# Performance work log

Hardware: AMD Instinct MI355X
Metric: run time of the kernel (lower is better)

Reference implementation:

```python
import jax, jax.numpy as jnp
import numpy as np

B, LQ, LV, D = 16, 2048, 2048, 1024


def setup_inputs() -> dict:
    key = jax.random.key(0)
    kq, kv = jax.random.split(key)
    query = jax.random.normal(kq, (B, LQ, D), dtype=jnp.float32)
    value = jax.random.normal(kv, (B, LV, D), dtype=jnp.float32)
    return {"query": query, "value": value}


def reference(query, value):
    # score: [B, Lq, Lv] -- unscaled dot-product attention (no 1/sqrt(d))
    score = jnp.einsum('bqd,bvd->bqv', query, value)
    attn = jax.nn.softmax(score, axis=-1)
    # dropout is identity in eval mode
    context = jnp.einsum('bqv,bvd->bqd', attn, value)
    return context
```

## Files before the change

kernel.cpp:

```cpp
#include <hip/hip_runtime.h>


#define B_ 16
#define LQ_ 2048
#define LV_ 2048
#define DD_ 1024

typedef unsigned short u16;
typedef _Float16 f16x8 __attribute__((ext_vector_type(8)));
typedef __attribute__((ext_vector_type(4))) float f32x4;
typedef __attribute__((ext_vector_type(4))) unsigned short u16x4;

__device__ __forceinline__ u16 f2h(float x) {
  union { _Float16 h; u16 u; } c;
  c.h = (_Float16)x;
  return c.u;
}

__device__ __forceinline__ void gload16(const u16* g, u16* lds) {
  __builtin_amdgcn_global_load_lds(
      (const __attribute__((address_space(1))) void*)g,
      (__attribute__((address_space(3))) void*)lds, 16, 0, 0);
}

#define BARRIER() do { asm volatile("" ::: "memory"); __builtin_amdgcn_s_barrier(); asm volatile("" ::: "memory"); } while (0)
#define WAITVM(N) asm volatile("s_waitcnt vmcnt(" #N ")" ::: "memory")

template <int TPS, int MODE>
__global__ __launch_bounds__(512, 2) void k_gemm8(
    const u16* __restrict__ A, const u16* __restrict__ B,
    u16* __restrict__ Pout, float* __restrict__ Fout,
    const u16* __restrict__ r2tab,
    float* __restrict__ mtab, float* __restrict__ stab,
    int N, int lda, int ldb, size_t aBatch, size_t bBatch, size_t cBatch) {
  constexpr int NT = TPS;
  __shared__ u16 lds[65536];
  __shared__ u16 ldsR2[(MODE == 2) ? 8192 : 64];
  u16* ldsA = lds;
  u16* ldsB = lds + 32768;

  int bx, by, bz;
  {
    const int gx = gridDim.x, gy = gridDim.y;
    const int lid = blockIdx.x + gx * (blockIdx.y + gy * blockIdx.z);
    const int nwg = gx * gy * gridDim.z;
    const int q = nwg >> 3;
    const int nid = (lid & 7) * q + (lid >> 3);
    bx = nid % gx;
    const int rem = nid / gx;
    by = rem % gy;
    bz = rem / gy;
  }

  const int tid = threadIdx.x;
  const int w = tid >> 6, l = tid & 63;
  const int m0 = by << 8, n0 = bx << 8;
  const int wr = w >> 2, wc = w & 3;
  const int wr128 = wr * 128, wc64 = wc * 64;
  const int fr = l & 15, kx = l >> 4, fr7 = l & 7, cc = l & 15;
  const int srow = l >> 3;
  const int gsrc8 = (((l & 7) ^ ((l >> 3) & 7)) << 3);

  const u16* Ab = A + (size_t)bz * aBatch;
  const u16* Bb = B + (size_t)bz * bBatch;

  if constexpr (MODE == 2) {
    for (int i = tid; i < 8192; i += 512)
      ldsR2[i] = r2tab[((size_t)bz * 32 + (i >> 8)) * 2048 + m0 + (i & 255)];
    __syncthreads();
  }

#define STAGE_A(tt, h)                                                          \
  do {                                                                          \
    const int kk_ = (tt) * 64;                                                  \
    u16* d0_ = ldsA + ((tt) & 1) * 16384 + ((h) * 64 + w * 8) * 64;             \
    const u16* g0_ = Ab + (size_t)(m0 + (h) * 64 + w * 8 + srow) * lda + kk_ + gsrc8; \
    gload16(g0_, d0_);                                                          \
    gload16(g0_ + (size_t)128 * lda, d0_ + 128 * 64);                           \
  } while (0)

#define STAGE_B(tt, h)                                                          \
  do {                                                                          \
    const int kk_ = (tt) * 64;                                                  \
    const int rb_ = (w >> 2) * 64 + (h) * 32 + (w & 3) * 8;                     \
    u16* d0_ = ldsB + ((tt) & 1) * 16384 + rb_ * 64;                            \
    const u16* g0_ = Bb + (size_t)(n0 + rb_ + srow) * ldb + kk_ + gsrc8;        \
    gload16(g0_, d0_);                                                          \
    gload16(g0_ + (size_t)128 * ldb, d0_ + 8192);                               \
  } while (0)

#define RA8(MOFF)                                                                   \
  {                                                                                 \
    _Pragma("unroll") for (int m_ = 0; m_ < 4; ++m_) {                              \
      _Pragma("unroll") for (int k_ = 0; k_ < 2; ++k_) {                            \
        af[m_][k_] = *(const f16x8*)(ldsA + bufo +                                  \
            (wr128 + (MOFF) + m_ * 16 + fr) * 64 + (((kx + k_ * 4) ^ fr7) << 3));   \
        if constexpr (MODE == 2) af[m_][k_] = af[m_][k_] * r2h[(MOFF) / 16 + m_];   \
      }                                                                             \
    }                                                                               \
  }

#define RB4(NF0)                                                                    \
  {                                                                                 \
    _Pragma("unroll") for (int n_ = 0; n_ < 2; ++n_) {                              \
      _Pragma("unroll") for (int k_ = 0; k_ < 2; ++k_) {                            \
        bf[(NF0) + n_][k_] = *(const f16x8*)(ldsB + bufo +                          \
            (wc64 + ((NF0) + n_) * 16 + fr) * 64 + (((kx + k_ * 4) ^ fr7) << 3));   \
      }                                                                             \
    }                                                                               \
  }

#define MFMA8(MF0, NF0)                                                             \
  {                                                                                 \
    _Pragma("unroll") for (int m_ = 0; m_ < 4; ++m_)                                \
    _Pragma("unroll") for (int n_ = 0; n_ < 2; ++n_)                                \
    _Pragma("unroll") for (int k_ = 0; k_ < 2; ++k_)                                \
        acc[(MF0) + m_][(NF0) + n_] = __builtin_amdgcn_mfma_f32_16x16x32_f16(       \
            af[m_][k_], bf[(NF0) + n_][k_], acc[(MF0) + m_][(NF0) + n_], 0, 0, 0);  \
  }

  f32x4 acc[8][4];
#pragma unroll
  for (int i = 0; i < 8; ++i)
#pragma unroll
    for (int j = 0; j < 4; ++j) acc[i][j] = (f32x4){0.f, 0.f, 0.f, 0.f};
  f16x8 af[4][2], bf[4][2];
  _Float16 r2h[8];

  STAGE_A(0, 0); STAGE_A(0, 1); STAGE_B(0, 0); STAGE_B(0, 1);
  STAGE_A(1, 0); STAGE_B(1, 0); STAGE_A(1, 1);
  WAITVM(6);
  BARRIER();

#pragma unroll 2
  for (int t = 0; t < NT; ++t) {
    const int bufo = (t & 1) * 16384;
    if constexpr (MODE == 2) {
#pragma unroll
      for (int i = 0; i < 8; ++i)
        r2h[i] = *(const _Float16*)&ldsR2[t * 256 + wr128 + i * 16 + fr];
    }
    RA8(0);
    RB4(0);
    if (t + 1 < NT) STAGE_B(t + 1, 1);
    BARRIER();
    __builtin_amdgcn_s_setprio(1); MFMA8(0, 0); __builtin_amdgcn_s_setprio(0);
    BARRIER();
    RB4(2);
    if (t + 2 < NT) STAGE_A(t + 2, 0);
    BARRIER();
    __builtin_amdgcn_s_setprio(1); MFMA8(0, 2); __builtin_amdgcn_s_setprio(0);
    BARRIER();
    RA8(64);
    if (t + 2 < NT) STAGE_B(t + 2, 0);
    BARRIER();
    __builtin_amdgcn_s_setprio(1); MFMA8(4, 0); __builtin_amdgcn_s_setprio(0);
    BARRIER();
    if (t + 2 < NT) STAGE_A(t + 2, 1);
    BARRIER();
    __builtin_amdgcn_s_setprio(1); MFMA8(4, 2); __builtin_amdgcn_s_setprio(0);
    if (t + 2 < NT) { WAITVM(6); } else if (t + 1 < NT) { WAITVM(0); }
    BARRIER();
  }

  const int rg4 = (l >> 4) * 4;
  if constexpr (MODE == 1) {
    u16* Pc = Pout + (size_t)bz * ((size_t)2048 * 2048);
    const int chunk = bx * 4 + wc;
    const size_t tbase = ((size_t)bz * 32 + chunk) * 2048 + m0;
#pragma unroll
    for (int mf = 0; mf < 8; ++mf) {
      float mt4[4], st4[4];
#pragma unroll
      for (int j = 0; j < 4; ++j) {
        const int r_ = wr128 + mf * 16 + rg4 + j;
        float v = fmaxf(fmaxf(acc[mf][0][j], acc[mf][1][j]),
                        fmaxf(acc[mf][2][j], acc[mf][3][j]));
#pragma unroll
        for (int off = 1; off < 16; off <<= 1) v = fmaxf(v, __shfl_xor(v, off, 64));
        const float e0 = __expf(acc[mf][0][j] - v);
        const float e1 = __expf(acc[mf][1][j] - v);
        const float e2 = __expf(acc[mf][2][j] - v);
        const float e3 = __expf(acc[mf][3][j] - v);
        u16* pr = Pc + (size_t)(m0 + r_) * 2048 + n0 + wc64 + cc;
        pr[0] = f2h(e0);
        pr[16] = f2h(e1);
        pr[32] = f2h(e2);
        pr[48] = f2h(e3);
        float s = (e0 + e1) + (e2 + e3);
#pragma unroll
        for (int off = 1; off < 16; off <<= 1) s += __shfl_xor(s, off, 64);
        mt4[j] = v;
        st4[j] = s;
      }
      if ((l & 15) == 0) {
        const int r0 = wr128 + mf * 16 + rg4;
        *(float4*)&mtab[tbase + r0] = make_float4(mt4[0], mt4[1], mt4[2], mt4[3]);
        *(float4*)&stab[tbase + r0] = make_float4(st4[0], st4[1], st4[2], st4[3]);
      }
    }
  } else {
#pragma unroll
    for (int mf = 0; mf < 8; ++mf)
#pragma unroll
      for (int nf = 0; nf < 4; ++nf) {
        float* cp = Fout + (size_t)bz * cBatch +
                    (size_t)(m0 + wr128 + mf * 16 + rg4) * N + n0 + wc64 + nf * 16 + cc;
#pragma unroll
        for (int j = 0; j < 4; ++j)
          cp[(size_t)j * N] = acc[mf][nf][j];
      }
  }
#undef STAGE_A
#undef STAGE_B
#undef RA8
#undef RB4
#undef MFMA8
}

__global__ __launch_bounds__(256) void k_stats(const float* __restrict__ mtab,
                                               const float* __restrict__ stab,
                                               u16* __restrict__ r2tab) {
  const int r = blockIdx.x * 256 + threadIdx.x;
  const int bz = blockIdx.y;
  float m[32], s[32], mg = -3.0e38f;
#pragma unroll
  for (int t = 0; t < 32; ++t) {
    m[t] = mtab[((size_t)bz * 32 + t) * 2048 + r];
    s[t] = stab[((size_t)bz * 32 + t) * 2048 + r];
    mg = fmaxf(mg, m[t]);
  }
  float denom = 0.f;
  float f[32];
#pragma unroll
  for (int t = 0; t < 32; ++t) {
    f[t] = __expf(m[t] - mg);
    denom += s[t] * f[t];
  }
  const float inv = 1.0f / denom;
#pragma unroll
  for (int t = 0; t < 32; ++t)
    r2tab[((size_t)bz * 32 + t) * 2048 + r] = f2h(f[t] * inv);
}

__global__ __launch_bounds__(256) void k_conv_q(const float* __restrict__ in,
                                                u16* __restrict__ hi_o, int nrows) {
  int t = blockIdx.x * 256 + threadIdx.x;
  int total = nrows * (DD_ / 4);
  if (t >= total) return;
  int row = t >> 8;
  int c4 = (t & 255) << 2;
  float4 v = *(const float4*)(in + (size_t)row * DD_ + c4);
  u16x4 hi;
  hi.x = f2h(v.x);
  hi.y = f2h(v.y);
  hi.z = f2h(v.z);
  hi.w = f2h(v.w);
  *(u16x4*)(hi_o + (size_t)row * DD_ + c4) = hi;
}

__global__ __launch_bounds__(256) void k_conv_vt(const float* __restrict__ V,
                                                 u16* __restrict__ Vh,
                                                 u16* __restrict__ VT) {
  __shared__ u16 tile[64][65];
  const int d0 = blockIdx.x * 64, v0 = blockIdx.y * 64;
  const size_t boff = (size_t)blockIdx.z * LV_ * DD_;
  const float* Vb = V + boff;
  u16* Vhb = Vh + boff;
  u16* VTb = VT + (size_t)blockIdx.z * DD_ * LV_;
  const int t = threadIdx.x;
  const int r = t >> 4, c4 = (t & 15) * 4;
#pragma unroll
  for (int i = 0; i < 4; ++i) {
    int row = r + i * 16;
    float4 x = *(const float4*)(Vb + (size_t)(v0 + row) * DD_ + d0 + c4);
    u16x4 h;
    h.x = f2h(x.x);
    h.y = f2h(x.y);
    h.z = f2h(x.z);
    h.w = f2h(x.w);
    *(u16x4*)(Vhb + (size_t)(v0 + row) * DD_ + d0 + c4) = h;
    tile[row][c4 + 0] = h.x;
    tile[row][c4 + 1] = h.y;
    tile[row][c4 + 2] = h.z;
    tile[row][c4 + 3] = h.w;
  }
  __syncthreads();
#pragma unroll
  for (int i = 0; i < 4; ++i) {
    int row = r + i * 16;
    u16x4 o;
    o.x = tile[c4 + 0][row];
    o.y = tile[c4 + 1][row];
    o.z = tile[c4 + 2][row];
    o.w = tile[c4 + 3][row];
    *(u16x4*)(VTb + (size_t)(d0 + row) * LV_ + v0 + c4) = o;
  }
}

extern "C" void kernel_launch(void* const* d_in, const int* in_sizes, int n_in,
                              void* d_out, int out_size, void* d_ws, size_t ws_size,
                              hipStream_t stream) {
  const float* Q = (const float*)d_in[0];
  const float* V = (const float*)d_in[1];
  float* out = (float*)d_out;

  const size_t qv_e = (size_t)LQ_ * DD_;
  const size_t vt_e = (size_t)DD_ * LV_;
  const size_t p_e = (size_t)LQ_ * LV_;
  const size_t tab_e = (size_t)32 * 2048;
  const size_t per_batch =
      qv_e * 2 * 2 + vt_e * 2 + p_e * 2 + tab_e * 4 * 2 + tab_e * 2;

  int nb = (int)(ws_size / per_batch);
  if (nb < 1) nb = 1;
  if (nb > B_) nb = B_;

  char* wp = (char*)d_ws;
  u16* Qh = (u16*)wp;    wp += (size_t)nb * qv_e * 2;
  u16* Vh = (u16*)wp;    wp += (size_t)nb * qv_e * 2;
  u16* VT = (u16*)wp;    wp += (size_t)nb * vt_e * 2;
  u16* P = (u16*)wp;     wp += (size_t)nb * p_e * 2;
  float* mtab = (float*)wp;  wp += (size_t)nb * tab_e * 4;
  float* stab = (float*)wp;  wp += (size_t)nb * tab_e * 4;
  u16* r2tab = (u16*)wp;

  for (int b0 = 0; b0 < B_; b0 += nb) {
    const int cb = (nb < B_ - b0) ? nb : (B_ - b0);
    const int rows = cb * LQ_;
    const int cthreads = rows * (DD_ / 4);
    k_conv_q<<<dim3((cthreads + 255) / 256), dim3(256), 0, stream>>>(
        Q + (size_t)b0 * LQ_ * DD_, Qh, rows);
    k_conv_vt<<<dim3(DD_ / 64, LV_ / 64, cb), dim3(256), 0, stream>>>(
        V + (size_t)b0 * LV_ * DD_, Vh, VT);
    k_gemm8<16, 1><<<dim3(LV_ / 256, LQ_ / 256, cb), dim3(512), 0, stream>>>(
        Qh, Vh, P, nullptr, nullptr, mtab, stab,
        LV_, DD_, DD_, qv_e, qv_e, 0);
    k_stats<<<dim3(LQ_ / 256, cb), dim3(256), 0, stream>>>(mtab, stab, r2tab);
    k_gemm8<32, 2><<<dim3(DD_ / 256, LQ_ / 256, cb), dim3(512), 0, stream>>>(
        P, VT, nullptr, out + (size_t)b0 * LQ_ * DD_, r2tab, nullptr, nullptr,
        DD_, LV_, LV_, p_e, vt_e, (size_t)LQ_ * DD_);
  }
}
```

Baseline: 416.1 us.

## Make GEMM workgroups loop over multiple N tiles with batch-per-XCD mapping

Each GEMM workgroup now walks several consecutive N tiles (4 for QK^T, 2 for PV) in one continuous K pipeline, running the softmax or store epilogue and clearing the accumulators at each tile boundary. Both launches shrink to a 2x8x16 grid. A new block mapping places whole batches on the same XCD, so A tiles and B panels stay in the local L2. The cost is half as many workgroups, so each CU may run only one 512-thread block instead of two, and the epilogue now sits inside the main loop where it can stall the pipeline.

```diff
diff --git a/kernel.cpp b/kernel.cpp
--- a/kernel.cpp
+++ b/kernel.cpp
@@ -26,35 +26,38 @@
 #define BARRIER() do { asm volatile("" ::: "memory"); __builtin_amdgcn_s_barrier(); asm volatile("" ::: "memory"); } while (0)
 #define WAITVM(N) asm volatile("s_waitcnt vmcnt(" #N ")" ::: "memory")
 
-template <int TPS, int MODE>
+template <int TPW, int TPS, int MODE>
 __global__ __launch_bounds__(512, 2) void k_gemm8(
     const u16* __restrict__ A, const u16* __restrict__ B,
     u16* __restrict__ Pout, float* __restrict__ Fout,
     const u16* __restrict__ r2tab,
     float* __restrict__ mtab, float* __restrict__ stab,
     int N, int lda, int ldb, size_t aBatch, size_t bBatch, size_t cBatch) {
-  constexpr int NT = TPS;
+  constexpr int NT = TPW * TPS;
   __shared__ u16 lds[65536];
   __shared__ u16 ldsR2[(MODE == 2) ? 8192 : 64];
   u16* ldsA = lds;
   u16* ldsB = lds + 32768;
 
   int bx, by, bz;
-  {
-    const int gx = gridDim.x, gy = gridDim.y;
-    const int lid = blockIdx.x + gx * (blockIdx.y + gy * blockIdx.z);
-    const int nwg = gx * gy * gridDim.z;
-    const int q = nwg >> 3;
-    const int nid = (lid & 7) * q + (lid >> 3);
-    bx = nid % gx;
-    const int rem = nid / gx;
-    by = rem % gy;
-    bz = rem / gy;
+  if (gridDim.z == 16 && gridDim.x == 2 && gridDim.y == 8) {
+    const int lid = blockIdx.x + 2 * (blockIdx.y + 8 * blockIdx.z);
+    const int xcd = lid & 7;
+    const int j = lid >> 3;
+    bz = xcd * 2 + (j >> 4);
+    const int r = j & 15;
+    by = r & 7;
+    bx = r >> 3;
+  } else {
+    bx = blockIdx.x;
+    by = blockIdx.y;
+    bz = blockIdx.z;
   }
 
   const int tid = threadIdx.x;
   const int w = tid >> 6, l = tid & 63;
-  const int m0 = by << 8, n0 = bx << 8;
+  const int m0 = by << 8;
+  const int n0base = bx * (TPW * 256);
   const int wr = w >> 2, wc = w & 3;
   const int wr128 = wr * 128, wc64 = wc * 64;
   const int fr = l & 15, kx = l >> 4, fr7 = l & 7, cc = l & 15;
@@ -72,7 +75,7 @@
 
 #define STAGE_A(tt, h)                                                          \
   do {                                                                          \
-    const int kk_ = (tt) * 64;                                                  \
+    const int kk_ = ((tt) % TPS) * 64;                                          \
     u16* d0_ = ldsA + ((tt) & 1) * 16384 + ((h) * 64 + w * 8) * 64;             \
     const u16* g0_ = Ab + (size_t)(m0 + (h) * 64 + w * 8 + srow) * lda + kk_ + gsrc8; \
     gload16(g0_, d0_);                                                          \
@@ -81,10 +84,11 @@
 
 #define STAGE_B(tt, h)                                                          \
   do {                                                                          \
-    const int kk_ = (tt) * 64;                                                  \
+    const int kk_ = ((tt) % TPS) * 64;                                          \
+    const int nb_ = n0base + ((tt) / TPS) * 256;                                \
     const int rb_ = (w >> 2) * 64 + (h) * 32 + (w & 3) * 8;                     \
     u16* d0_ = ldsB + ((tt) & 1) * 16384 + rb_ * 64;                            \
-    const u16* g0_ = Bb + (size_t)(n0 + rb_ + srow) * ldb + kk_ + gsrc8;        \
+    const u16* g0_ = Bb + (size_t)(nb_ + rb_ + srow) * ldb + kk_ + gsrc8;       \
     gload16(g0_, d0_);                                                          \
     gload16(g0_ + (size_t)128 * ldb, d0_ + 8192);                               \
   } while (0)
@@ -127,6 +131,8 @@
   f16x8 af[4][2], bf[4][2];
   _Float16 r2h[8];
 
+  const int rg4 = (l >> 4) * 4;
+
   STAGE_A(0, 0); STAGE_A(0, 1); STAGE_B(0, 0); STAGE_B(0, 1);
   STAGE_A(1, 0); STAGE_B(1, 0); STAGE_A(1, 1);
   WAITVM(6);
@@ -136,9 +142,10 @@
   for (int t = 0; t < NT; ++t) {
     const int bufo = (t & 1) * 16384;
     if constexpr (MODE == 2) {
+      const int chb = (t & (TPS - 1)) * 256;
 #pragma unroll
       for (int i = 0; i < 8; ++i)
-        r2h[i] = *(const _Float16*)&ldsR2[t * 256 + wr128 + i * 16 + fr];
+        r2h[i] = *(const _Float16*)&ldsR2[chb + wr128 + i * 16 + fr];
     }
     RA8(0);
     RB4(0);
@@ -161,55 +168,61 @@
     __builtin_amdgcn_s_setprio(1); MFMA8(4, 2); __builtin_amdgcn_s_setprio(0);
     if (t + 2 < NT) { WAITVM(6); } else if (t + 1 < NT) { WAITVM(0); }
     BARRIER();
-  }
-
-  const int rg4 = (l >> 4) * 4;
-  if constexpr (MODE == 1) {
-    u16* Pc = Pout + (size_t)bz * ((size_t)2048 * 2048);
-    const int chunk = bx * 4 + wc;
-    const size_t tbase = ((size_t)bz * 32 + chunk) * 2048 + m0;
-#pragma unroll
-    for (int mf = 0; mf < 8; ++mf) {
-      float mt4[4], st4[4];
-#pragma unroll
-      for (int j = 0; j < 4; ++j) {
-        const int r_ = wr128 + mf * 16 + rg4 + j;
-        float v = fmaxf(fmaxf(acc[mf][0][j], acc[mf][1][j]),
-                        fmaxf(acc[mf][2][j], acc[mf][3][j]));
-#pragma unroll
-        for (int off = 1; off < 16; off <<= 1) v = fmaxf(v, __shfl_xor(v, off, 64));
-        const float e0 = __expf(acc[mf][0][j] - v);
-        const float e1 = __expf(acc[mf][1][j] - v);
-        const float e2 = __expf(acc[mf][2][j] - v);
-        const float e3 = __expf(acc[mf][3][j] - v);
-        u16* pr = Pc + (size_t)(m0 + r_) * 2048 + n0 + wc64 + cc;
-        pr[0] = f2h(e0);
-        pr[16] = f2h(e1);
-        pr[32] = f2h(e2);
-        pr[48] = f2h(e3);
-        float s = (e0 + e1) + (e2 + e3);
-#pragma unroll
-        for (int off = 1; off < 16; off <<= 1) s += __shfl_xor(s, off, 64);
-        mt4[j] = v;
-        st4[j] = s;
+
+    if ((t & (TPS - 1)) == (TPS - 1)) {
+      const int n0c = n0base + (t / TPS) * 256;
+      if constexpr (MODE == 1) {
+        u16* Pc = Pout + (size_t)bz * ((size_t)2048 * 2048);
+        const int chunk = (n0c >> 6) + wc;
+        const size_t tbase = ((size_t)bz * 32 + chunk) * 2048 + m0;
+#pragma unroll
+        for (int mf = 0; mf < 8; ++mf) {
+          float mt4[4], st4[4];
+#pragma unroll
+          for (int j = 0; j < 4; ++j) {
+            const int r_ = wr128 + mf * 16 + rg4 + j;
+            float v = fmaxf(fmaxf(acc[mf][0][j], acc[mf][1][j]),
+                            fmaxf(acc[mf][2][j], acc[mf][3][j]));
+#pragma unroll
+            for (int off = 1; off < 16; off <<= 1) v = fmaxf(v, __shfl_xor(v, off, 64));
+            const float e0 = __expf(acc[mf][0][j] - v);
+            const float e1 = __expf(acc[mf][1][j] - v);
+            const float e2 = __expf(acc[mf][2][j] - v);
+            const float e3 = __expf(acc[mf][3][j] - v);
+            u16* pr = Pc + (size_t)(m0 + r_) * 2048 + n0c + wc64 + cc;
+            pr[0] = f2h(e0);
+            pr[16] = f2h(e1);
+            pr[32] = f2h(e2);
+            pr[48] = f2h(e3);
+            float s = (e0 + e1) + (e2 + e3);
+#pragma unroll
+            for (int off = 1; off < 16; off <<= 1) s += __shfl_xor(s, off, 64);
+            mt4[j] = v;
+            st4[j] = s;
+          }
+          if ((l & 15) == 0) {
+            const int r0 = wr128 + mf * 16 + rg4;
+            *(float4*)&mtab[tbase + r0] = make_float4(mt4[0], mt4[1], mt4[2], mt4[3]);
+            *(float4*)&stab[tbase + r0] = make_float4(st4[0], st4[1], st4[2], st4[3]);
+          }
+        }
+      } else {
+#pragma unroll
+        for (int mf = 0; mf < 8; ++mf)
+#pragma unroll
+          for (int nf = 0; nf < 4; ++nf) {
+            float* cp = Fout + (size_t)bz * cBatch +
+                        (size_t)(m0 + wr128 + mf * 16 + rg4) * N + n0c + wc64 + nf * 16 + cc;
+#pragma unroll
+            for (int j = 0; j < 4; ++j)
+              cp[(size_t)j * N] = acc[mf][nf][j];
+          }
       }
-      if ((l & 15) == 0) {
-        const int r0 = wr128 + mf * 16 + rg4;
-        *(float4*)&mtab[tbase + r0] = make_float4(mt4[0], mt4[1], mt4[2], mt4[3]);
-        *(float4*)&stab[tbase + r0] = make_float4(st4[0], st4[1], st4[2], st4[3]);
-      }
+#pragma unroll
+      for (int i = 0; i < 8; ++i)
+#pragma unroll
+        for (int j = 0; j < 4; ++j) acc[i][j] = (f32x4){0.f, 0.f, 0.f, 0.f};
     }
-  } else {
-#pragma unroll
-    for (int mf = 0; mf < 8; ++mf)
-#pragma unroll
-      for (int nf = 0; nf < 4; ++nf) {
-        float* cp = Fout + (size_t)bz * cBatch +
-                    (size_t)(m0 + wr128 + mf * 16 + rg4) * N + n0 + wc64 + nf * 16 + cc;
-#pragma unroll
-        for (int j = 0; j < 4; ++j)
-          cp[(size_t)j * N] = acc[mf][nf][j];
-      }
   }
 #undef STAGE_A
 #undef STAGE_B
@@ -333,11 +346,11 @@
         Q + (size_t)b0 * LQ_ * DD_, Qh, rows);
     k_conv_vt<<<dim3(DD_ / 64, LV_ / 64, cb), dim3(256), 0, stream>>>(
         V + (size_t)b0 * LV_ * DD_, Vh, VT);
-    k_gemm8<16, 1><<<dim3(LV_ / 256, LQ_ / 256, cb), dim3(512), 0, stream>>>(
+    k_gemm8<4, 16, 1><<<dim3(2, 8, cb), dim3(512), 0, stream>>>(
         Qh, Vh, P, nullptr, nullptr, mtab, stab,
         LV_, DD_, DD_, qv_e, qv_e, 0);
     k_stats<<<dim3(LQ_ / 256, cb), dim3(256), 0, stream>>>(mtab, stab, r2tab);
-    k_gemm8<32, 2><<<dim3(DD_ / 256, LQ_ / 256, cb), dim3(512), 0, stream>>>(
+    k_gemm8<2, 32, 2><<<dim3(2, 8, cb), dim3(512), 0, stream>>>(
         P, VT, nullptr, out + (size_t)b0 * LQ_ * DD_, r2tab, nullptr, nullptr,
         DD_, LV_, LV_, p_e, vt_e, (size_t)LQ_ * DD_);
   }
```

Measured after the change: 431.3 us. 1.04x slower.

## Replace pipelined 256x256 GEMM with simple 128x128 single-buffered GEMM

Applied to the files above, without the earlier changes.

Replaces the 512-thread, 256x256-tile GEMM with a 256-thread, 128x128-tile GEMM. The old kernel double-buffered 64-wide K slabs, interleaved loads with MFMA phases and raised wave priority around the MFMAs. The new kernel stages 32-wide K slabs through a single LDS buffer with two __syncthreads per step and a new XOR swizzle, and launches at 4 blocks per CU. The smaller tile and LDS footprint aim to raise occupancy and simplify the code. In exchange it gives up load/compute overlap and halves per-block data reuse, so it needs more global traffic and synchronisation per FLOP.

```diff
diff --git a/kernel.cpp b/kernel.cpp
--- a/kernel.cpp
+++ b/kernel.cpp
@@ -23,21 +23,16 @@
       (__attribute__((address_space(3))) void*)lds, 16, 0, 0);
 }
 
-#define BARRIER() do { asm volatile("" ::: "memory"); __builtin_amdgcn_s_barrier(); asm volatile("" ::: "memory"); } while (0)
-#define WAITVM(N) asm volatile("s_waitcnt vmcnt(" #N ")" ::: "memory")
-
-template <int TPS, int MODE>
-__global__ __launch_bounds__(512, 2) void k_gemm8(
+template <int K, int MODE>
+__global__ __launch_bounds__(256, 4) void k_gemm(
     const u16* __restrict__ A, const u16* __restrict__ B,
     u16* __restrict__ Pout, float* __restrict__ Fout,
     const u16* __restrict__ r2tab,
     float* __restrict__ mtab, float* __restrict__ stab,
     int N, int lda, int ldb, size_t aBatch, size_t bBatch, size_t cBatch) {
-  constexpr int NT = TPS;
-  __shared__ u16 lds[65536];
-  __shared__ u16 ldsR2[(MODE == 2) ? 8192 : 64];
-  u16* ldsA = lds;
-  u16* ldsB = lds + 32768;
+  __shared__ u16 ldsA[128 * 32];
+  __shared__ u16 ldsB[128 * 32];
+  __shared__ u16 ldsR2[(MODE == 2) ? (K / 64) * 128 : 64];
 
   int bx, by, bz;
   {
@@ -54,126 +49,78 @@
 
   const int tid = threadIdx.x;
   const int w = tid >> 6, l = tid & 63;
-  const int m0 = by << 8, n0 = bx << 8;
-  const int wr = w >> 2, wc = w & 3;
-  const int wr128 = wr * 128, wc64 = wc * 64;
-  const int fr = l & 15, kx = l >> 4, fr7 = l & 7, cc = l & 15;
-  const int srow = l >> 3;
-  const int gsrc8 = (((l & 7) ^ ((l >> 3) & 7)) << 3);
+  const int m0 = by << 7, n0 = bx << 7;
+  const int wr64 = (w >> 1) * 64, wc64 = (w & 1) * 64;
+  const int fr = l & 15, kx = l >> 4;
+  const int rg4 = kx * 4, cc = fr;
+  const int gsw = ((kx ^ ((fr ^ (fr >> 2)) & 3)) << 3);
+  const int rd = tid >> 2, gd = tid & 3;
+  const int gsA0 = ((gd ^ ((rd ^ (rd >> 2)) & 3)) << 3);
+  const int rd1 = rd + 64;
+  const int gsA1 = ((gd ^ ((rd1 ^ (rd1 >> 2)) & 3)) << 3);
 
   const u16* Ab = A + (size_t)bz * aBatch;
   const u16* Bb = B + (size_t)bz * bBatch;
 
   if constexpr (MODE == 2) {
-    for (int i = tid; i < 8192; i += 512)
-      ldsR2[i] = r2tab[((size_t)bz * 32 + (i >> 8)) * 2048 + m0 + (i & 255)];
+    for (int i = tid; i < (K / 64) * 128; i += 256)
+      ldsR2[i] = r2tab[((size_t)bz * 32 + (i >> 7)) * 2048 + m0 + (i & 127)];
     __syncthreads();
   }
 
-#define STAGE_A(tt, h)                                                          \
-  do {                                                                          \
-    const int kk_ = (tt) * 64;                                                  \
-    u16* d0_ = ldsA + ((tt) & 1) * 16384 + ((h) * 64 + w * 8) * 64;             \
-    const u16* g0_ = Ab + (size_t)(m0 + (h) * 64 + w * 8 + srow) * lda + kk_ + gsrc8; \
-    gload16(g0_, d0_);                                                          \
-    gload16(g0_ + (size_t)128 * lda, d0_ + 128 * 64);                           \
-  } while (0)
-
-#define STAGE_B(tt, h)                                                          \
-  do {                                                                          \
-    const int kk_ = (tt) * 64;                                                  \
-    const int rb_ = (w >> 2) * 64 + (h) * 32 + (w & 3) * 8;                     \
-    u16* d0_ = ldsB + ((tt) & 1) * 16384 + rb_ * 64;                            \
-    const u16* g0_ = Bb + (size_t)(n0 + rb_ + srow) * ldb + kk_ + gsrc8;        \
-    gload16(g0_, d0_);                                                          \
-    gload16(g0_ + (size_t)128 * ldb, d0_ + 8192);                               \
-  } while (0)
-
-#define RA8(MOFF)                                                                   \
-  {                                                                                 \
-    _Pragma("unroll") for (int m_ = 0; m_ < 4; ++m_) {                              \
-      _Pragma("unroll") for (int k_ = 0; k_ < 2; ++k_) {                            \
-        af[m_][k_] = *(const f16x8*)(ldsA + bufo +                                  \
-            (wr128 + (MOFF) + m_ * 16 + fr) * 64 + (((kx + k_ * 4) ^ fr7) << 3));   \
-        if constexpr (MODE == 2) af[m_][k_] = af[m_][k_] * r2h[(MOFF) / 16 + m_];   \
-      }                                                                             \
-    }                                                                               \
-  }
-
-#define RB4(NF0)                                                                    \
-  {                                                                                 \
-    _Pragma("unroll") for (int n_ = 0; n_ < 2; ++n_) {                              \
-      _Pragma("unroll") for (int k_ = 0; k_ < 2; ++k_) {                            \
-        bf[(NF0) + n_][k_] = *(const f16x8*)(ldsB + bufo +                          \
-            (wc64 + ((NF0) + n_) * 16 + fr) * 64 + (((kx + k_ * 4) ^ fr7) << 3));   \
-      }                                                                             \
-    }                                                                               \
-  }
-
-#define MFMA8(MF0, NF0)                                                             \
-  {                                                                                 \
-    _Pragma("unroll") for (int m_ = 0; m_ < 4; ++m_)                                \
-    _Pragma("unroll") for (int n_ = 0; n_ < 2; ++n_)                                \
-    _Pragma("unroll") for (int k_ = 0; k_ < 2; ++k_)                                \
-        acc[(MF0) + m_][(NF0) + n_] = __builtin_amdgcn_mfma_f32_16x16x32_f16(       \
-            af[m_][k_], bf[(NF0) + n_][k_], acc[(MF0) + m_][(NF0) + n_], 0, 0, 0);  \
-  }
-
-  f32x4 acc[8][4];
-#pragma unroll
-  for (int i = 0; i < 8; ++i)
+  f32x4 acc[4][4];
+#pragma unroll
+  for (int i = 0; i < 4; ++i)
 #pragma unroll
     for (int j = 0; j < 4; ++j) acc[i][j] = (f32x4){0.f, 0.f, 0.f, 0.f};
-  f16x8 af[4][2], bf[4][2];
-  _Float16 r2h[8];
-
-  STAGE_A(0, 0); STAGE_A(0, 1); STAGE_B(0, 0); STAGE_B(0, 1);
-  STAGE_A(1, 0); STAGE_B(1, 0); STAGE_A(1, 1);
-  WAITVM(6);
-  BARRIER();
-
-#pragma unroll 2
-  for (int t = 0; t < NT; ++t) {
-    const int bufo = (t & 1) * 16384;
+  f16x8 af[4], bf[4];
+  _Float16 r2h[4];
+
+  for (int kt = 0; kt < K; kt += 32) {
+    {
+      const u16* ga = Ab + (size_t)(m0 + rd) * lda + kt;
+      const u16* gb = Bb + (size_t)(n0 + rd) * ldb + kt;
+      gload16(ga + gsA0, &ldsA[rd * 32 + gd * 8]);
+      gload16(ga + (size_t)64 * lda + gsA1, &ldsA[rd1 * 32 + gd * 8]);
+      gload16(gb + gsA0, &ldsB[rd * 32 + gd * 8]);
+      gload16(gb + (size_t)64 * ldb + gsA1, &ldsB[rd1 * 32 + gd * 8]);
+    }
+    __syncthreads();
     if constexpr (MODE == 2) {
-#pragma unroll
-      for (int i = 0; i < 8; ++i)
-        r2h[i] = *(const _Float16*)&ldsR2[t * 256 + wr128 + i * 16 + fr];
-    }
-    RA8(0);
-    RB4(0);
-    if (t + 1 < NT) STAGE_B(t + 1, 1);
-    BARRIER();
-    __builtin_amdgcn_s_setprio(1); MFMA8(0, 0); __builtin_amdgcn_s_setprio(0);
-    BARRIER();
-    RB4(2);
-    if (t + 2 < NT) STAGE_A(t + 2, 0);
-    BARRIER();
-    __builtin_amdgcn_s_setprio(1); MFMA8(0, 2); __builtin_amdgcn_s_setprio(0);
-    BARRIER();
-    RA8(64);
-    if (t + 2 < NT) STAGE_B(t + 2, 0);
-    BARRIER();
-    __builtin_amdgcn_s_setprio(1); MFMA8(4, 0); __builtin_amdgcn_s_setprio(0);
-    BARRIER();
-    if (t + 2 < NT) STAGE_A(t + 2, 1);
-    BARRIER();
-    __builtin_amdgcn_s_setprio(1); MFMA8(4, 2); __builtin_amdgcn_s_setprio(0);
-    if (t + 2 < NT) { WAITVM(6); } else if (t + 1 < NT) { WAITVM(0); }
-    BARRIER();
-  }
-
-  const int rg4 = (l >> 4) * 4;
+      if ((kt & 63) == 0) {
+        const int chb = (kt >> 6) * 128;
+#pragma unroll
+        for (int m_ = 0; m_ < 4; ++m_)
+          r2h[m_] = *(const _Float16*)&ldsR2[chb + wr64 + m_ * 16 + fr];
+      }
+    }
+#pragma unroll
+    for (int m_ = 0; m_ < 4; ++m_) {
+      af[m_] = *(const f16x8*)&ldsA[(wr64 + m_ * 16 + fr) * 32 + gsw];
+      if constexpr (MODE == 2) af[m_] = af[m_] * r2h[m_];
+    }
+#pragma unroll
+    for (int n_ = 0; n_ < 4; ++n_)
+      bf[n_] = *(const f16x8*)&ldsB[(wc64 + n_ * 16 + fr) * 32 + gsw];
+#pragma unroll
+    for (int m_ = 0; m_ < 4; ++m_)
+#pragma unroll
+      for (int n_ = 0; n_ < 4; ++n_)
+        acc[m_][n_] = __builtin_amdgcn_mfma_f32_16x16x32_f16(
+            af[m_], bf[n_], acc[m_][n_], 0, 0, 0);
+    __syncthreads();
+  }
+
   if constexpr (MODE == 1) {
     u16* Pc = Pout + (size_t)bz * ((size_t)2048 * 2048);
-    const int chunk = bx * 4 + wc;
+    const int chunk = bx * 2 + (w & 1);
     const size_t tbase = ((size_t)bz * 32 + chunk) * 2048 + m0;
 #pragma unroll
-    for (int mf = 0; mf < 8; ++mf) {
+    for (int mf = 0; mf < 4; ++mf) {
       float mt4[4], st4[4];
 #pragma unroll
       for (int j = 0; j < 4; ++j) {
-        const int r_ = wr128 + mf * 16 + rg4 + j;
+        const int r_ = wr64 + mf * 16 + rg4 + j;
         float v = fmaxf(fmaxf(acc[mf][0][j], acc[mf][1][j]),
                         fmaxf(acc[mf][2][j], acc[mf][3][j]));
 #pragma unroll
@@ -194,28 +141,22 @@
         st4[j] = s;
       }
       if ((l & 15) == 0) {
-        const int r0 = wr128 + mf * 16 + rg4;
+        const int r0 = wr64 + mf * 16 + rg4;
         *(float4*)&mtab[tbase + r0] = make_float4(mt4[0], mt4[1], mt4[2], mt4[3]);
         *(float4*)&stab[tbase + r0] = make_float4(st4[0], st4[1], st4[2], st4[3]);
       }
     }
   } else {
-#pragma unroll
-    for (int mf = 0; mf < 8; ++mf)
+    float* Cb = Fout + (size_t)bz * cBatch;
+#pragma unroll
+    for (int mf = 0; mf < 4; ++mf)
 #pragma unroll
       for (int nf = 0; nf < 4; ++nf) {
-        float* cp = Fout + (size_t)bz * cBatch +
-                    (size_t)(m0 + wr128 + mf * 16 + rg4) * N + n0 + wc64 + nf * 16 + cc;
-#pragma unroll
-        for (int j = 0; j < 4; ++j)
-          cp[(size_t)j * N] = acc[mf][nf][j];
-      }
-  }
-#undef STAGE_A
-#undef STAGE_B
-#undef RA8
-#undef RB4
-#undef MFMA8
+        float* cp = Cb + (size_t)(m0 + wr64 + mf * 16 + rg4) * N + n0 + wc64 + nf * 16 + cc;
+#pragma unroll
+        for (int j = 0; j < 4; ++j) cp[(size_t)j * N] = acc[mf][nf][j];
+      }
+  }
 }
 
 __global__ __launch_bounds__(256) void k_stats(const float* __restrict__ mtab,
@@ -333,11 +274,11 @@
         Q + (size_t)b0 * LQ_ * DD_, Qh, rows);
     k_conv_vt<<<dim3(DD_ / 64, LV_ / 64, cb), dim3(256), 0, stream>>>(
         V + (size_t)b0 * LV_ * DD_, Vh, VT);
-    k_gemm8<16, 1><<<dim3(LV_ / 256, LQ_ / 256, cb), dim3(512), 0, stream>>>(
+    k_gemm<1024, 1><<<dim3(LV_ / 128, LQ_ / 128, cb), dim3(256), 0, stream>>>(
         Qh, Vh, P, nullptr, nullptr, mtab, stab,
         LV_, DD_, DD_, qv_e, qv_e, 0);
     k_stats<<<dim3(LQ_ / 256, cb), dim3(256), 0, stream>>>(mtab, stab, r2tab);
-    k_gemm8<32, 2><<<dim3(DD_ / 256, LQ_ / 256, cb), dim3(512), 0, stream>>>(
+    k_gemm<2048, 2><<<dim3(DD_ / 128, LQ_ / 128, cb), dim3(256), 0, stream>>>(
         P, VT, nullptr, out + (size_t)b0 * LQ_ * DD_, r2tab, nullptr, nullptr,
         DD_, LV_, LV_, p_e, vt_e, (size_t)LQ_ * DD_);
   }
```

Measured after the change: 455.9 us. 9.6% more time.

## Fuse softmax stats into second GEMM and make first GEMM persistent over two M tiles

Applied to the files above, without the earlier changes.

Removes the separate k_stats kernel: the second GEMM's prologue now reduces the per-chunk max and sum tables directly into LDS rescale factors. The first GEMM is restructured so each workgroup walks two consecutive 256-row M tiles, with the epilogue moved inside the loop so it runs at each tile boundary and staging continues across tiles. This cuts a kernel launch and the r2tab round trip, and lets the pipeline stay primed between tiles. The cost is fewer workgroups for the first GEMM and serial per-row work by 256 threads in each second-GEMM workgroup prologue. The fp16 round trip of the factors before multiplying by inv may change rounding slightly.

```diff
diff --git a/kernel.cpp b/kernel.cpp
--- a/kernel.cpp
+++ b/kernel.cpp
@@ -16,6 +16,11 @@
   c.h = (_Float16)x;
   return c.u;
 }
+__device__ __forceinline__ float h2f(u16 u) {
+  union { _Float16 h; u16 u; } c;
+  c.u = u;
+  return (float)c.h;
+}
 
 __device__ __forceinline__ void gload16(const u16* g, u16* lds) {
   __builtin_amdgcn_global_load_lds(
@@ -26,14 +31,13 @@
 #define BARRIER() do { asm volatile("" ::: "memory"); __builtin_amdgcn_s_barrier(); asm volatile("" ::: "memory"); } while (0)
 #define WAITVM(N) asm volatile("s_waitcnt vmcnt(" #N ")" ::: "memory")
 
-template <int TPS, int MODE>
+template <int TPW, int TPS, int MODE>
 __global__ __launch_bounds__(512, 2) void k_gemm8(
     const u16* __restrict__ A, const u16* __restrict__ B,
     u16* __restrict__ Pout, float* __restrict__ Fout,
-    const u16* __restrict__ r2tab,
     float* __restrict__ mtab, float* __restrict__ stab,
     int N, int lda, int ldb, size_t aBatch, size_t bBatch, size_t cBatch) {
-  constexpr int NT = TPS;
+  constexpr int NT = TPW * TPS;
   __shared__ u16 lds[65536];
   __shared__ u16 ldsR2[(MODE == 2) ? 8192 : 64];
   u16* ldsA = lds;
@@ -54,7 +58,8 @@
 
   const int tid = threadIdx.x;
   const int w = tid >> 6, l = tid & 63;
-  const int m0 = by << 8, n0 = bx << 8;
+  const int m0base = by * (TPW * 256);
+  const int n0 = bx << 8;
   const int wr = w >> 2, wc = w & 3;
   const int wr128 = wr * 128, wc64 = wc * 64;
   const int fr = l & 15, kx = l >> 4, fr7 = l & 7, cc = l & 15;
@@ -65,23 +70,40 @@
   const u16* Bb = B + (size_t)bz * bBatch;
 
   if constexpr (MODE == 2) {
-    for (int i = tid; i < 8192; i += 512)
-      ldsR2[i] = r2tab[((size_t)bz * 32 + (i >> 8)) * 2048 + m0 + (i & 255)];
+    if (tid < 256) {
+      const int r = tid;
+      const size_t base = (size_t)bz * 32 * 2048 + m0base + r;
+      float mg = -3.0e38f;
+#pragma unroll
+      for (int c = 0; c < 32; ++c) mg = fmaxf(mg, mtab[base + (size_t)c * 2048]);
+      float denom = 0.f;
+#pragma unroll
+      for (int c = 0; c < 32; ++c) {
+        const float f = __expf(mtab[base + (size_t)c * 2048] - mg);
+        denom += stab[base + (size_t)c * 2048] * f;
+        ldsR2[c * 256 + r] = f2h(f);
+      }
+      const float inv = 1.0f / denom;
+#pragma unroll
+      for (int c = 0; c < 32; ++c)
+        ldsR2[c * 256 + r] = f2h(h2f(ldsR2[c * 256 + r]) * inv);
+    }
     __syncthreads();
   }
 
 #define STAGE_A(tt, h)                                                          \
   do {                                                                          \
-    const int kk_ = (tt) * 64;                                                  \
+    const int kk_ = ((tt) % TPS) * 64;                                          \
+    const int ma_ = m0base + ((tt) / TPS) * 256;                                \
     u16* d0_ = ldsA + ((tt) & 1) * 16384 + ((h) * 64 + w * 8) * 64;             \
-    const u16* g0_ = Ab + (size_t)(m0 + (h) * 64 + w * 8 + srow) * lda + kk_ + gsrc8; \
+    const u16* g0_ = Ab + (size_t)(ma_ + (h) * 64 + w * 8 + srow) * lda + kk_ + gsrc8; \
     gload16(g0_, d0_);                                                          \
     gload16(g0_ + (size_t)128 * lda, d0_ + 128 * 64);                           \
   } while (0)
 
 #define STAGE_B(tt, h)                                                          \
   do {                                                                          \
-    const int kk_ = (tt) * 64;                                                  \
+    const int kk_ = ((tt) % TPS) * 64;                                          \
     const int rb_ = (w >> 2) * 64 + (h) * 32 + (w & 3) * 8;                     \
     u16* d0_ = ldsB + ((tt) & 1) * 16384 + rb_ * 64;                            \
     const u16* g0_ = Bb + (size_t)(n0 + rb_ + srow) * ldb + kk_ + gsrc8;        \
@@ -127,6 +149,8 @@
   f16x8 af[4][2], bf[4][2];
   _Float16 r2h[8];
 
+  const int rg4 = (l >> 4) * 4;
+
   STAGE_A(0, 0); STAGE_A(0, 1); STAGE_B(0, 0); STAGE_B(0, 1);
   STAGE_A(1, 0); STAGE_B(1, 0); STAGE_A(1, 1);
   WAITVM(6);
@@ -136,9 +160,10 @@
   for (int t = 0; t < NT; ++t) {
     const int bufo = (t & 1) * 16384;
     if constexpr (MODE == 2) {
+      const int chb = (t & (TPS - 1)) * 256;
 #pragma unroll
       for (int i = 0; i < 8; ++i)
-        r2h[i] = *(const _Float16*)&ldsR2[t * 256 + wr128 + i * 16 + fr];
+        r2h[i] = *(const _Float16*)&ldsR2[chb + wr128 + i * 16 + fr];
     }
     RA8(0);
     RB4(0);
@@ -161,86 +186,69 @@
     __builtin_amdgcn_s_setprio(1); MFMA8(4, 2); __builtin_amdgcn_s_setprio(0);
     if (t + 2 < NT) { WAITVM(6); } else if (t + 1 < NT) { WAITVM(0); }
     BARRIER();
-  }
-
-  const int rg4 = (l >> 4) * 4;
-  if constexpr (MODE == 1) {
-    u16* Pc = Pout + (size_t)bz * ((size_t)2048 * 2048);
-    const int chunk = bx * 4 + wc;
-    const size_t tbase = ((size_t)bz * 32 + chunk) * 2048 + m0;
-#pragma unroll
-    for (int mf = 0; mf < 8; ++mf) {
-      float mt4[4], st4[4];
-#pragma unroll
-      for (int j = 0; j < 4; ++j) {
-        const int r_ = wr128 + mf * 16 + rg4 + j;
-        float v = fmaxf(fmaxf(acc[mf][0][j], acc[mf][1][j]),
-                        fmaxf(acc[mf][2][j], acc[mf][3][j]));
-#pragma unroll
-        for (int off = 1; off < 16; off <<= 1) v = fmaxf(v, __shfl_xor(v, off, 64));
-        const float e0 = __expf(acc[mf][0][j] - v);
-        const float e1 = __expf(acc[mf][1][j] - v);
-        const float e2 = __expf(acc[mf][2][j] - v);
-        const float e3 = __expf(acc[mf][3][j] - v);
-        u16* pr = Pc + (size_t)(m0 + r_) * 2048 + n0 + wc64 + cc;
-        pr[0] = f2h(e0);
-        pr[16] = f2h(e1);
-        pr[32] = f2h(e2);
-        pr[48] = f2h(e3);
-        float s = (e0 + e1) + (e2 + e3);
-#pragma unroll
-        for (int off = 1; off < 16; off <<= 1) s += __shfl_xor(s, off, 64);
-        mt4[j] = v;
-        st4[j] = s;
+
+    if ((t & (TPS - 1)) == (TPS - 1)) {
+      const int m0c = m0base + (t / TPS) * 256;
+      if constexpr (MODE == 1) {
+        u16* Pc = Pout + (size_t)bz * ((size_t)2048 * 2048);
+        const int chunk = (n0 >> 6) + wc;
+        const size_t tbase = ((size_t)bz * 32 + chunk) * 2048 + m0c;
+#pragma unroll
+        for (int mf = 0; mf < 8; ++mf) {
+          float mt4[4], st4[4];
+#pragma unroll
+          for (int j = 0; j < 4; ++j) {
+            const int r_ = wr128 + mf * 16 + rg4 + j;
+            float v = fmaxf(fmaxf(acc[mf][0][j], acc[mf][1][j]),
+                            fmaxf(acc[mf][2][j], acc[mf][3][j]));
+#pragma unroll
+            for (int off = 1; off < 16; off <<= 1) v = fmaxf(v, __shfl_xor(v, off, 64));
+            const float e0 = __expf(acc[mf][0][j] - v);
+            const float e1 = __expf(acc[mf][1][j] - v);
+            const float e2 = __expf(acc[mf][2][j] - v);
+            const float e3 = __expf(acc[mf][3][j] - v);
+            u16* pr = Pc + (size_t)(m0c + r_) * 2048 + n0 + wc64 + cc;
+            pr[0] = f2h(e0);
+            pr[16] = f2h(e1);
+            pr[32] = f2h(e2);
+            pr[48] = f2h(e3);
+            float s = (e0 + e1) + (e2 + e3);
+#pragma unroll
+            for (int off = 1; off < 16; off <<= 1) s += __shfl_xor(s, off, 64);
+            mt4[j] = v;
+            st4[j] = s;
+          }
+          if ((l & 15) == 0) {
+            const int r0 = wr128 + mf * 16 + rg4;
+            *(float4*)&mtab[tbase + r0] = make_float4(mt4[0], mt4[1], mt4[2], mt4[3]);
+            *(float4*)&stab[tbase + r0] = make_float4(st4[0], st4[1], st4[2], st4[3]);
+          }
+        }
+      } else {
+#pragma unroll
+        for (int mf = 0; mf < 8; ++mf)
+#pragma unroll
+          for (int nf = 0; nf < 4; ++nf) {
+            float* cp = Fout + (size_t)bz * cBatch +
+                        (size_t)(m0c + wr128 + mf * 16 + rg4) * N + n0 + wc64 + nf * 16 + cc;
+#pragma unroll
+            for (int j = 0; j < 4; ++j)
+              cp[(size_t)j * N] = acc[mf][nf][j];
+          }
       }
-      if ((l & 15) == 0) {
-        const int r0 = wr128 + mf * 16 + rg4;
-        *(float4*)&mtab[tbase + r0] = make_float4(mt4[0], mt4[1], mt4[2], mt4[3]);
-        *(float4*)&stab[tbase + r0] = make_float4(st4[0], st4[1], st4[2], st4[3]);
+      if (t + 1 < NT) {
+#pragma unroll
+        for (int i = 0; i < 8; ++i)
+#pragma unroll
+          for (int j = 0; j < 4; ++j) acc[i][j] = (f32x4){0.f, 0.f, 0.f, 0.f};
       }
     }
-  } else {
-#pragma unroll
-    for (int mf = 0; mf < 8; ++mf)
-#pragma unroll
-      for (int nf = 0; nf < 4; ++nf) {
-        float* cp = Fout + (size_t)bz * cBatch +
-                    (size_t)(m0 + wr128 + mf * 16 + rg4) * N + n0 + wc64 + nf * 16 + cc;
-#pragma unroll
-        for (int j = 0; j < 4; ++j)
-          cp[(size_t)j * N] = acc[mf][nf][j];
-      }
   }
 #undef STAGE_A
 #undef STAGE_B
 #undef RA8
 #undef RB4
 #undef MFMA8
-}
-
-__global__ __launch_bounds__(256) void k_stats(const float* __restrict__ mtab,
-                                               const float* __restrict__ stab,
-                                               u16* __restrict__ r2tab) {
-  const int r = blockIdx.x * 256 + threadIdx.x;
-  const int bz = blockIdx.y;
-  float m[32], s[32], mg = -3.0e38f;
-#pragma unroll
-  for (int t = 0; t < 32; ++t) {
-    m[t] = mtab[((size_t)bz * 32 + t) * 2048 + r];
-    s[t] = stab[((size_t)bz * 32 + t) * 2048 + r];
-    mg = fmaxf(mg, m[t]);
-  }
-  float denom = 0.f;
-  float f[32];
-#pragma unroll
-  for (int t = 0; t < 32; ++t) {
-    f[t] = __expf(m[t] - mg);
-    denom += s[t] * f[t];
-  }
-  const float inv = 1.0f / denom;
-#pragma unroll
-  for (int t = 0; t < 32; ++t)
-    r2tab[((size_t)bz * 32 + t) * 2048 + r] = f2h(f[t] * inv);
 }
 
 __global__ __launch_bounds__(256) void k_conv_q(const float* __restrict__ in,
@@ -310,7 +318,7 @@
   const size_t p_e = (size_t)LQ_ * LV_;
   const size_t tab_e = (size_t)32 * 2048;
   const size_t per_batch =
-      qv_e * 2 * 2 + vt_e * 2 + p_e * 2 + tab_e * 4 * 2 + tab_e * 2;
+      qv_e * 2 * 2 + vt_e * 2 + p_e * 2 + tab_e * 4 * 2;
 
   int nb = (int)(ws_size / per_batch);
   if (nb < 1) nb = 1;
@@ -322,8 +330,7 @@
   u16* VT = (u16*)wp;    wp += (size_t)nb * vt_e * 2;
   u16* P = (u16*)wp;     wp += (size_t)nb * p_e * 2;
   float* mtab = (float*)wp;  wp += (size_t)nb * tab_e * 4;
-  float* stab = (float*)wp;  wp += (size_t)nb * tab_e * 4;
-  u16* r2tab = (u16*)wp;
+  float* stab = (float*)wp;
 
   for (int b0 = 0; b0 < B_; b0 += nb) {
     const int cb = (nb < B_ - b0) ? nb : (B_ - b0);
@@ -333,12 +340,11 @@
         Q + (size_t)b0 * LQ_ * DD_, Qh, rows);
     k_conv_vt<<<dim3(DD_ / 64, LV_ / 64, cb), dim3(256), 0, stream>>>(
         V + (size_t)b0 * LV_ * DD_, Vh, VT);
-    k_gemm8<16, 1><<<dim3(LV_ / 256, LQ_ / 256, cb), dim3(512), 0, stream>>>(
-        Qh, Vh, P, nullptr, nullptr, mtab, stab,
+    k_gemm8<2, 16, 1><<<dim3(LV_ / 256, LQ_ / 512, cb), dim3(512), 0, stream>>>(
+        Qh, Vh, P, nullptr, mtab, stab,
         LV_, DD_, DD_, qv_e, qv_e, 0);
-    k_stats<<<dim3(LQ_ / 256, cb), dim3(256), 0, stream>>>(mtab, stab, r2tab);
-    k_gemm8<32, 2><<<dim3(DD_ / 256, LQ_ / 256, cb), dim3(512), 0, stream>>>(
-        P, VT, nullptr, out + (size_t)b0 * LQ_ * DD_, r2tab, nullptr, nullptr,
+    k_gemm8<1, 32, 2><<<dim3(DD_ / 256, LQ_ / 256, cb), dim3(512), 0, stream>>>(
+        P, VT, nullptr, out + (size_t)b0 * LQ_ * DD_, mtab, stab,
         DD_, LV_, LV_, p_e, vt_e, (size_t)LQ_ * DD_);
   }
 }
```

New measurement: 520.3 us. 1.25x slower.
